# Kernel tuning notes

Measured on AMD Instinct MI355X. Metric: run time of the kernel, lower is better.

## Reference

```python
import jax, jax.numpy as jnp
import numpy as np

N, D, H = 65536, 512, 256  # batch, input_dim, hidden_dim
BN_EPS = 1e-5
EPS = 1e-15


def setup_inputs() -> dict:
    key = jax.random.key(0)
    ks = jax.random.split(key, 10)
    rn = lambda k, shape, sc: jax.random.normal(k, shape, dtype=jnp.float32) * sc
    return {
        "x1": rn(ks[0], (N, D), 1.0),
        "x2": rn(ks[1], (N, D), 1.0),
        "W1": rn(ks[2], (D, H), 0.04),
        "b1": jnp.zeros((H,), jnp.float32),
        "gamma": jnp.ones((H,), jnp.float32),
        "beta_bn": jnp.zeros((H,), jnp.float32),
        "W2": rn(ks[3], (H, H // 2), 0.06),
        "b2": jnp.zeros((H // 2,), jnp.float32),
        "W3": rn(ks[4], (H // 2 * 3, 64), 0.05),
        "b3": jnp.zeros((64,), jnp.float32),
        "W4": rn(ks[5], (64, 1), 0.12),
        "b4": jnp.zeros((1,), jnp.float32),
        "alpha": jnp.array([0.65], jnp.float32),
        "beta": jnp.array([0.25], jnp.float32),
    }


def _proj(x, W1, b1, gamma, beta_bn, W2, b2):
    h = x @ W1 + b1                       # [N, 256]
    mean = jnp.mean(h, axis=0)
    var = jnp.var(h, axis=0)              # biased, matches BN training normalization
    h = gamma * (h - mean) * jax.lax.rsqrt(var + BN_EPS) + beta_bn
    h = jax.nn.relu(h)
    return jax.nn.relu(h @ W2 + b2)       # [N, 128]


def reference(x1, x2, W1, b1, gamma, beta_bn, W2, b2, W3, b3, W4, b4, alpha, beta):
    h1 = _proj(x1, W1, b1, gamma, beta_bn, W2, b2)
    h2 = _proj(x2, W1, b1, gamma, beta_bn, W2, b2)
    # diag of normalized similarity matrix == row-wise cosine similarity
    dot = jnp.sum(h1 * h2, axis=1)
    inv1 = 1.0 / jnp.maximum(jnp.sqrt(jnp.sum(h1 * h1, axis=1)), EPS)
    inv2 = 1.0 / jnp.maximum(jnp.sqrt(jnp.sum(h2 * h2, axis=1)), EPS)
    s_math = jnp.clip(dot * inv1 * inv2, 0.0, 1.0)
    combined = jnp.concatenate([h1 * h2, jnp.abs(h1 - h2), h1 + h2], axis=1)  # [N, 384]
    s_learn = (jax.nn.relu(combined @ W3 + b3) @ W4 + b4).reshape(-1)          # [N]
    final = alpha * s_math + beta * jax.nn.sigmoid(s_learn)
    return jnp.clip(final, 0.0, 1.0)
```

## Files before the change

kernel.cpp:

```cpp
#include <hip/hip_runtime.h>
#include <hip/hip_bf16.h>
#include <math.h>

#define NROWS 65536
#define DIN   512
#define H1    256
#define H2    128
#define K3DIM 384
#define O3    64

typedef short  short8  __attribute__((ext_vector_type(8)));
typedef float  f32x4   __attribute__((ext_vector_type(4)));
typedef unsigned short u16x4 __attribute__((ext_vector_type(4)));

__device__ __forceinline__ unsigned short f2bf(float f) {
    union { float f; unsigned int i; } v; v.f = f;
    unsigned int r = (v.i + 0x7fffu + ((v.i >> 16) & 1u)) >> 16;
    return (unsigned short)r;
}
__device__ __forceinline__ float bf2f(unsigned short u) {
    union { unsigned int i; float f; } v; v.i = ((unsigned int)u) << 16;
    return v.f;
}

typedef const __attribute__((address_space(1))) unsigned int* gas1_t;
typedef __attribute__((address_space(3))) unsigned int* las3_t;
__device__ __forceinline__ void gload_lds16(const void* g, void* l) {
    __builtin_amdgcn_global_load_lds((gas1_t)g, (las3_t)l, 16, 0, 0);
}

__global__ void transpose3_kernel(const float* __restrict__ W1, const float* __restrict__ W2,
                                  const float* __restrict__ W3,
                                  unsigned short* __restrict__ w1t, unsigned short* __restrict__ w2t,
                                  unsigned short* __restrict__ w3t) {
    int idx = blockIdx.x * 256 + threadIdx.x;
    const int n1 = DIN * H1;
    const int n2 = H1 * H2;
    const int n3 = K3DIM * O3;
    if (idx < n1) {
        int c = idx / DIN, r = idx - c * DIN;
        w1t[idx] = f2bf(W1[r * H1 + c]);
    } else if (idx < n1 + n2) {
        int i2 = idx - n1;
        int c = i2 / H1, r = i2 - c * H1;
        w2t[i2] = f2bf(W2[r * H2 + c]);
    } else if (idx < n1 + n2 + n3) {
        int i3 = idx - n1 - n2;
        int c = i3 / K3DIM, r = i3 - c * K3DIM;
        w3t[i3] = f2bf(W3[r * O3 + c]);
    }
}

#define LDA1 32

__global__ __launch_bounds__(256, 2)
void gemm1_kernel(const float* __restrict__ x1, const float* __restrict__ x2,
                  const unsigned short* __restrict__ w1t, const float* __restrict__ b1,
                  unsigned short* __restrict__ h_out, float* __restrict__ stats) {
    __shared__ __align__(1024) unsigned short Al[2][64 * LDA1];
    __shared__ __align__(1024) unsigned short Bl[2][256 * LDA1];
    const int t    = threadIdx.x;
    const int row0 = blockIdx.x * 64;
    const int inp  = row0 >> 16;
    const float* xp = inp ? x2 : x1;
    const int r0 = row0 & (NROWS - 1);

    const int wave = t >> 6, lane = t & 63;
    const int m = lane & 15, q = lane >> 4;

    const int bn_local = lane >> 2;
    const int bk_off   = (lane & 3) * 8;
    const int ar0 = t >> 3;
    const int ak0 = (t & 7) * 4;

    f32x4 acc[4][4] = {};
    float4 va0, va1;

#pragma unroll
    for (int i = 0; i < 4; ++i) {
        int chunk = wave * 4 + i;
        gload_lds16(w1t + (size_t)(chunk * 16 + bn_local) * DIN + bk_off, &Bl[0][chunk * 512]);
    }
    va0 = *reinterpret_cast<const float4*>(xp + (size_t)(r0 + ar0) * DIN + ak0);
    va1 = *reinterpret_cast<const float4*>(xp + (size_t)(r0 + ar0 + 32) * DIN + ak0);
    {
        u16x4 c0; c0.x = f2bf(va0.x); c0.y = f2bf(va0.y); c0.z = f2bf(va0.z); c0.w = f2bf(va0.w);
        u16x4 c1; c1.x = f2bf(va1.x); c1.y = f2bf(va1.y); c1.z = f2bf(va1.z); c1.w = f2bf(va1.w);
        *reinterpret_cast<u16x4*>(&Al[0][ar0 * LDA1 + ak0])        = c0;
        *reinterpret_cast<u16x4*>(&Al[0][(ar0 + 32) * LDA1 + ak0]) = c1;
    }
    __syncthreads();

#pragma unroll
    for (int kt = 0; kt < 16; ++kt) {
        const int d = kt & 1;
        if (kt < 15) {
            const int kn = (kt + 1) * 32;
#pragma unroll
            for (int i = 0; i < 4; ++i) {
                int chunk = wave * 4 + i;
                gload_lds16(w1t + (size_t)(chunk * 16 + bn_local) * DIN + kn + bk_off,
                            &Bl[d ^ 1][chunk * 512]);
            }
            va0 = *reinterpret_cast<const float4*>(xp + (size_t)(r0 + ar0) * DIN + kn + ak0);
            va1 = *reinterpret_cast<const float4*>(xp + (size_t)(r0 + ar0 + 32) * DIN + kn + ak0);
        }
        short8 af[4], bfr[4];
#pragma unroll
        for (int mi = 0; mi < 4; ++mi)
            af[mi] = *reinterpret_cast<const short8*>(&Al[d][(mi * 16 + m) * LDA1 + q * 8]);
#pragma unroll
        for (int ni = 0; ni < 4; ++ni)
            bfr[ni] = *reinterpret_cast<const short8*>(&Bl[d][(wave * 64 + ni * 16 + m) * LDA1 + q * 8]);
#pragma unroll
        for (int mi = 0; mi < 4; ++mi)
#pragma unroll
            for (int ni = 0; ni < 4; ++ni)
                acc[mi][ni] = __builtin_amdgcn_mfma_f32_16x16x32_bf16(af[mi], bfr[ni], acc[mi][ni], 0, 0, 0);
        if (kt < 15) {
            u16x4 c0; c0.x = f2bf(va0.x); c0.y = f2bf(va0.y); c0.z = f2bf(va0.z); c0.w = f2bf(va0.w);
            u16x4 c1; c1.x = f2bf(va1.x); c1.y = f2bf(va1.y); c1.z = f2bf(va1.z); c1.w = f2bf(va1.w);
            *reinterpret_cast<u16x4*>(&Al[d ^ 1][ar0 * LDA1 + ak0])        = c0;
            *reinterpret_cast<u16x4*>(&Al[d ^ 1][(ar0 + 32) * LDA1 + ak0]) = c1;
        }
        __syncthreads();
    }

#pragma unroll
    for (int ni = 0; ni < 4; ++ni) {
        const int col = wave * 64 + ni * 16 + m;
        const float bias = b1[col];
        float s = 0.f, ssq = 0.f;
#pragma unroll
        for (int mi = 0; mi < 4; ++mi) {
#pragma unroll
            for (int r = 0; r < 4; ++r) {
                int row = row0 + mi * 16 + q * 4 + r;
                float v = acc[mi][ni][r] + bias;
                h_out[(size_t)row * H1 + col] = f2bf(v);
                s += v; ssq += v * v;
            }
        }
        s   += __shfl_xor(s, 16);   s   += __shfl_xor(s, 32);
        ssq += __shfl_xor(ssq, 16); ssq += __shfl_xor(ssq, 32);
        if (q == 0) {
            atomicAdd(&stats[(inp * 2 + 0) * H1 + col], s);
            atomicAdd(&stats[(inp * 2 + 1) * H1 + col], ssq);
        }
    }
}

__global__ void bnparams_kernel(const float* __restrict__ stats, const float* __restrict__ gamma,
                                const float* __restrict__ beta_bn, float* __restrict__ ab) {
    int t = threadIdx.x;
    int inp = t >> 8, c = t & 255;
    float mean = stats[(inp * 2 + 0) * H1 + c] * (1.0f / NROWS);
    float ex2  = stats[(inp * 2 + 1) * H1 + c] * (1.0f / NROWS);
    float var  = ex2 - mean * mean;
    float a = gamma[c] * rsqrtf(var + 1e-5f);
    ab[(inp * 2 + 0) * H1 + c] = a;
    ab[(inp * 2 + 1) * H1 + c] = beta_bn[c] - a * mean;
}

#define LDA  40

__global__ __launch_bounds__(256, 2)
void gemm2_kernel(const unsigned short* __restrict__ h, const unsigned short* __restrict__ w2t,
                  const float* __restrict__ b2, const float* __restrict__ ab,
                  unsigned short* __restrict__ z) {
    __shared__ __align__(16) unsigned short Al[2][128 * LDA];
    __shared__ float sc[H1], sh[H1];
    const int t  = threadIdx.x;
    const int m0 = blockIdx.x * 128;
    const int inp = m0 >> 16;
    sc[t] = ab[(inp * 2 + 0) * H1 + t];
    sh[t] = ab[(inp * 2 + 1) * H1 + t];

    const int wave = t >> 6, lane = t & 63;
    const int wm = wave >> 1, wn = wave & 1;
    const int m = lane & 15, q = lane >> 4;
    const int ar = t >> 1, akh = (t & 1) * 16;
    const unsigned short* hrow = h + (size_t)(m0 + ar) * H1 + akh;

    f32x4 acc[4][4] = {};
    short8 bcur[4], bnext[4];
    float4 ha0, ha1;

    ha0 = *reinterpret_cast<const float4*>(hrow);
    ha1 = *reinterpret_cast<const float4*>(hrow + 8);
#pragma unroll
    for (int ni = 0; ni < 4; ++ni)
        bcur[ni] = *reinterpret_cast<const short8*>(w2t + (size_t)(wn * 64 + ni * 16 + m) * H1 + q * 8);
    __syncthreads();
    {
        unsigned short vs[16] __attribute__((aligned(16)));
        unsigned short ob[16] __attribute__((aligned(16)));
        *reinterpret_cast<float4*>(vs)     = ha0;
        *reinterpret_cast<float4*>(vs + 8) = ha1;
#pragma unroll
        for (int j = 0; j < 16; ++j) {
            float v = sc[akh + j] * bf2f(vs[j]) + sh[akh + j];
            ob[j] = f2bf(fmaxf(v, 0.f));
        }
        *reinterpret_cast<float4*>(&Al[0][ar * LDA + akh])     = *reinterpret_cast<float4*>(ob);
        *reinterpret_cast<float4*>(&Al[0][ar * LDA + akh + 8]) = *reinterpret_cast<float4*>(ob + 8);
    }
    __syncthreads();

#pragma unroll
    for (int kt = 0; kt < 8; ++kt) {
        const int d = kt & 1;
        if (kt < 7) {
            const int kn = (kt + 1) * 32;
            ha0 = *reinterpret_cast<const float4*>(hrow + kn);
            ha1 = *reinterpret_cast<const float4*>(hrow + kn + 8);
#pragma unroll
            for (int ni = 0; ni < 4; ++ni)
                bnext[ni] = *reinterpret_cast<const short8*>(
                    w2t + (size_t)(wn * 64 + ni * 16 + m) * H1 + kn + q * 8);
        }
        short8 af[4];
#pragma unroll
        for (int mi = 0; mi < 4; ++mi)
            af[mi] = *reinterpret_cast<const short8*>(&Al[d][(wm * 64 + mi * 16 + m) * LDA + q * 8]);
#pragma unroll
        for (int mi = 0; mi < 4; ++mi)
#pragma unroll
            for (int ni = 0; ni < 4; ++ni)
                acc[mi][ni] = __builtin_amdgcn_mfma_f32_16x16x32_bf16(af[mi], bcur[ni], acc[mi][ni], 0, 0, 0);
        if (kt < 7) {
            const int kn = (kt + 1) * 32;
            unsigned short vs[16] __attribute__((aligned(16)));
            unsigned short ob[16] __attribute__((aligned(16)));
            *reinterpret_cast<float4*>(vs)     = ha0;
            *reinterpret_cast<float4*>(vs + 8) = ha1;
#pragma unroll
            for (int j = 0; j < 16; ++j) {
                int k = kn + akh + j;
                float v = sc[k] * bf2f(vs[j]) + sh[k];
                ob[j] = f2bf(fmaxf(v, 0.f));
            }
            *reinterpret_cast<float4*>(&Al[d ^ 1][ar * LDA + akh])     = *reinterpret_cast<float4*>(ob);
            *reinterpret_cast<float4*>(&Al[d ^ 1][ar * LDA + akh + 8]) = *reinterpret_cast<float4*>(ob + 8);
#pragma unroll
            for (int ni = 0; ni < 4; ++ni) bcur[ni] = bnext[ni];
        }
        __syncthreads();
    }
#pragma unroll
    for (int mi = 0; mi < 4; ++mi)
#pragma unroll
        for (int ni = 0; ni < 4; ++ni) {
            int col = wn * 64 + ni * 16 + m;
            float bias = b2[col];
#pragma unroll
            for (int r = 0; r < 4; ++r) {
                int row = m0 + wm * 64 + mi * 16 + q * 4 + r;
                z[(size_t)row * H2 + col] = f2bf(fmaxf(acc[mi][ni][r] + bias, 0.f));
            }
        }
}

#define LDZ  136

__global__ __launch_bounds__(512, 2)
void head_kernel(const unsigned short* __restrict__ z, const unsigned short* __restrict__ w3t,
                 const float* __restrict__ b3, const float* __restrict__ w4,
                 const float* __restrict__ b4, const float* __restrict__ alpha,
                 const float* __restrict__ beta, float* __restrict__ out) {
    __shared__ __align__(16) unsigned short Z1[128 * LDZ];
    __shared__ __align__(16) unsigned short Z2[128 * LDZ];
    __shared__ float b3s[64], w4s[64];
    __shared__ float smath[128], slearn[128];

    const int t  = threadIdx.x;
    const int r0 = blockIdx.x * 128;

    {
        int r = t >> 2, seg = t & 3;
        const float4* f1 = reinterpret_cast<const float4*>(z + (size_t)(r0 + r) * H2 + seg * 32);
        const float4* f2 = reinterpret_cast<const float4*>(z + (size_t)(NROWS + r0 + r) * H2 + seg * 32);
        float4* d1 = reinterpret_cast<float4*>(&Z1[r * LDZ + seg * 32]);
        float4* d2 = reinterpret_cast<float4*>(&Z2[r * LDZ + seg * 32]);
        d1[0] = f1[0]; d1[1] = f1[1]; d1[2] = f1[2]; d1[3] = f1[3];
        d2[0] = f2[0]; d2[1] = f2[1]; d2[2] = f2[2]; d2[3] = f2[3];
    }
    if (t < 64) { b3s[t] = b3[t]; w4s[t] = w4[t]; }
    __syncthreads();

    {
        int r = t >> 2, part = t & 3;
        float d = 0.f, s1 = 0.f, s2 = 0.f;
#pragma unroll
        for (int j = 0; j < 32; ++j) {
            int k = part * 32 + j;
            float a = bf2f(Z1[r * LDZ + k]);
            float b = bf2f(Z2[r * LDZ + k]);
            d += a * b; s1 += a * a; s2 += b * b;
        }
        d  += __shfl_xor(d, 1);  d  += __shfl_xor(d, 2);
        s1 += __shfl_xor(s1, 1); s1 += __shfl_xor(s1, 2);
        s2 += __shfl_xor(s2, 1); s2 += __shfl_xor(s2, 2);
        if (part == 0) {
            float inv1 = 1.f / fmaxf(sqrtf(s1), 1e-15f);
            float inv2 = 1.f / fmaxf(sqrtf(s2), 1e-15f);
            float sm = d * inv1 * inv2;
            smath[r] = fminf(fmaxf(sm, 0.f), 1.f);
        }
    }

    const int wave = t >> 6, lane = t & 63;
    const int m = lane & 15, q = lane >> 4;
    const int wr = wave * 16;
    f32x4 acc[4] = {};
#pragma unroll
    for (int kb = 0; kb < 12; ++kb) {
        int seg = kb >> 2;
        int kl  = (kb & 3) * 32 + q * 8;
        short8 a1 = *reinterpret_cast<const short8*>(&Z1[(wr + m) * LDZ + kl]);
        short8 a2 = *reinterpret_cast<const short8*>(&Z2[(wr + m) * LDZ + kl]);
        short8 af;
#pragma unroll
        for (int j = 0; j < 8; ++j) {
            float v1 = bf2f((unsigned short)a1[j]);
            float v2 = bf2f((unsigned short)a2[j]);
            float v = (seg == 0) ? v1 * v2 : (seg == 1 ? fabsf(v1 - v2) : v1 + v2);
            af[j] = (short)f2bf(v);
        }
#pragma unroll
        for (int ni = 0; ni < 4; ++ni) {
            short8 bfr = *reinterpret_cast<const short8*>(
                w3t + (size_t)(ni * 16 + m) * K3DIM + kb * 32 + q * 8);
            acc[ni] = __builtin_amdgcn_mfma_f32_16x16x32_bf16(af, bfr, acc[ni], 0, 0, 0);
        }
    }
    float partial[4] = {0.f, 0.f, 0.f, 0.f};
#pragma unroll
    for (int ni = 0; ni < 4; ++ni) {
        int col = ni * 16 + m;
        float bias = b3s[col], w4v = w4s[col];
#pragma unroll
        for (int rg = 0; rg < 4; ++rg) {
            float v = fmaxf(acc[ni][rg] + bias, 0.f);
            partial[rg] += v * w4v;
        }
    }
#pragma unroll
    for (int rg = 0; rg < 4; ++rg) {
        float p = partial[rg];
        p += __shfl_xor(p, 1); p += __shfl_xor(p, 2);
        p += __shfl_xor(p, 4); p += __shfl_xor(p, 8);
        if (m == 0) slearn[wr + q * 4 + rg] = p + b4[0];
    }
    __syncthreads();
    if (t < 128) {
        float sl = slearn[t];
        float sig = 1.f / (1.f + expf(-sl));
        float f = alpha[0] * smath[t] + beta[0] * sig;
        out[r0 + t] = fminf(fmaxf(f, 0.f), 1.f);
    }
}

extern "C" void kernel_launch(void* const* d_in, const int* in_sizes, int n_in,
                              void* d_out, int out_size, void* d_ws, size_t ws_size,
                              hipStream_t stream) {
    (void)in_sizes; (void)n_in; (void)out_size; (void)ws_size;
    const float* x1      = (const float*)d_in[0];
    const float* x2      = (const float*)d_in[1];
    const float* W1      = (const float*)d_in[2];
    const float* b1      = (const float*)d_in[3];
    const float* gamma   = (const float*)d_in[4];
    const float* beta_bn = (const float*)d_in[5];
    const float* W2      = (const float*)d_in[6];
    const float* b2      = (const float*)d_in[7];
    const float* W3      = (const float*)d_in[8];
    const float* b3      = (const float*)d_in[9];
    const float* W4      = (const float*)d_in[10];
    const float* b4      = (const float*)d_in[11];
    const float* alpha   = (const float*)d_in[12];
    const float* beta    = (const float*)d_in[13];
    float* out = (float*)d_out;

    char* ws = (char*)d_ws;
    unsigned short* h   = (unsigned short*)(ws);
    unsigned short* w1t = (unsigned short*)(ws + 67108864);
    unsigned short* w2t = (unsigned short*)(ws + 67371008);
    unsigned short* w3t = (unsigned short*)(ws + 67436544);
    float*          stats = (float*)(ws + 67485696);
    float*          ab    = (float*)(ws + 67489792);
    unsigned short* z   = (unsigned short*)(ws + 67493888);

    (void)hipMemsetAsync(stats, 0, 4096, stream);
    transpose3_kernel<<<(DIN * H1 + H1 * H2 + K3DIM * O3 + 255) / 256, 256, 0, stream>>>(
        W1, W2, W3, w1t, w2t, w3t);
    gemm1_kernel<<<2048, 256, 0, stream>>>(x1, x2, w1t, b1, h, stats);
    bnparams_kernel<<<1, 512, 0, stream>>>(stats, gamma, beta_bn, ab);
    gemm2_kernel<<<1024, 256, 0, stream>>>(h, w2t, b2, ab, z);
    head_kernel<<<512, 512, 0, stream>>>(z, w3t, b3, W4, b4, alpha, beta, out);
}
```

Before: 420.5 us.

## Use single-buffered BK=64 tiles with XOR-swizzled LDS for gemm1 and gemm2

Both GEMMs drop register/LDS double buffering and instead stage 64-wide K tiles in one LDS buffer, with two syncs per tile. B tiles are loaded directly into LDS through global_load_lds with an XOR swizzle to avoid bank conflicts. gemm2 now also stages W2 through LDS rather than reading it from global memory into registers. This halves the number of K iterations and cuts bank conflicts, but it gives up overlap of loads with MFMA work inside a block and relies on the two blocks per CU to hide latency.

```diff
diff --git a/kernel.cpp b/kernel.cpp
--- a/kernel.cpp
+++ b/kernel.cpp
@@ -11,7 +11,6 @@
 
 typedef short  short8  __attribute__((ext_vector_type(8)));
 typedef float  f32x4   __attribute__((ext_vector_type(4)));
-typedef unsigned short u16x4 __attribute__((ext_vector_type(4)));
 
 __device__ __forceinline__ unsigned short f2bf(float f) {
     union { float f; unsigned int i; } v; v.f = f;
@@ -51,84 +50,78 @@
     }
 }
 
-#define LDA1 32
+#define LDA1P 72
 
 __global__ __launch_bounds__(256, 2)
 void gemm1_kernel(const float* __restrict__ x1, const float* __restrict__ x2,
                   const unsigned short* __restrict__ w1t, const float* __restrict__ b1,
                   unsigned short* __restrict__ h_out, float* __restrict__ stats) {
-    __shared__ __align__(1024) unsigned short Al[2][64 * LDA1];
-    __shared__ __align__(1024) unsigned short Bl[2][256 * LDA1];
+    __shared__ __align__(1024) unsigned short Bl[256 * 64];
+    __shared__ __align__(16)   unsigned short Al[64 * LDA1P];
     const int t    = threadIdx.x;
     const int row0 = blockIdx.x * 64;
     const int inp  = row0 >> 16;
     const float* xp = inp ? x2 : x1;
     const int r0 = row0 & (NROWS - 1);
 
-    const int wave = t >> 6, lane = t & 63;
+    const int w = t >> 6, lane = t & 63;
     const int m = lane & 15, q = lane >> 4;
 
-    const int bn_local = lane >> 2;
-    const int bk_off   = (lane & 3) * 8;
-    const int ar0 = t >> 3;
-    const int ak0 = (t & 7) * 4;
+    const int brow_l = lane >> 3;
+    const int bslot  = (lane & 7) ^ brow_l;
+    const int arow  = t >> 2;
+    const int akseg = (t & 3) * 16;
 
     f32x4 acc[4][4] = {};
-    float4 va0, va1;
-
-#pragma unroll
-    for (int i = 0; i < 4; ++i) {
-        int chunk = wave * 4 + i;
-        gload_lds16(w1t + (size_t)(chunk * 16 + bn_local) * DIN + bk_off, &Bl[0][chunk * 512]);
-    }
-    va0 = *reinterpret_cast<const float4*>(xp + (size_t)(r0 + ar0) * DIN + ak0);
-    va1 = *reinterpret_cast<const float4*>(xp + (size_t)(r0 + ar0 + 32) * DIN + ak0);
-    {
-        u16x4 c0; c0.x = f2bf(va0.x); c0.y = f2bf(va0.y); c0.z = f2bf(va0.z); c0.w = f2bf(va0.w);
-        u16x4 c1; c1.x = f2bf(va1.x); c1.y = f2bf(va1.y); c1.z = f2bf(va1.z); c1.w = f2bf(va1.w);
-        *reinterpret_cast<u16x4*>(&Al[0][ar0 * LDA1 + ak0])        = c0;
-        *reinterpret_cast<u16x4*>(&Al[0][(ar0 + 32) * LDA1 + ak0]) = c1;
-    }
-    __syncthreads();
-
-#pragma unroll
-    for (int kt = 0; kt < 16; ++kt) {
-        const int d = kt & 1;
-        if (kt < 15) {
-            const int kn = (kt + 1) * 32;
-#pragma unroll
-            for (int i = 0; i < 4; ++i) {
-                int chunk = wave * 4 + i;
-                gload_lds16(w1t + (size_t)(chunk * 16 + bn_local) * DIN + kn + bk_off,
-                            &Bl[d ^ 1][chunk * 512]);
-            }
-            va0 = *reinterpret_cast<const float4*>(xp + (size_t)(r0 + ar0) * DIN + kn + ak0);
-            va1 = *reinterpret_cast<const float4*>(xp + (size_t)(r0 + ar0 + 32) * DIN + kn + ak0);
-        }
-        short8 af[4], bfr[4];
-#pragma unroll
-        for (int mi = 0; mi < 4; ++mi)
-            af[mi] = *reinterpret_cast<const short8*>(&Al[d][(mi * 16 + m) * LDA1 + q * 8]);
-#pragma unroll
-        for (int ni = 0; ni < 4; ++ni)
-            bfr[ni] = *reinterpret_cast<const short8*>(&Bl[d][(wave * 64 + ni * 16 + m) * LDA1 + q * 8]);
-#pragma unroll
-        for (int mi = 0; mi < 4; ++mi)
-#pragma unroll
-            for (int ni = 0; ni < 4; ++ni)
-                acc[mi][ni] = __builtin_amdgcn_mfma_f32_16x16x32_bf16(af[mi], bfr[ni], acc[mi][ni], 0, 0, 0);
-        if (kt < 15) {
-            u16x4 c0; c0.x = f2bf(va0.x); c0.y = f2bf(va0.y); c0.z = f2bf(va0.z); c0.w = f2bf(va0.w);
-            u16x4 c1; c1.x = f2bf(va1.x); c1.y = f2bf(va1.y); c1.z = f2bf(va1.z); c1.w = f2bf(va1.w);
-            *reinterpret_cast<u16x4*>(&Al[d ^ 1][ar0 * LDA1 + ak0])        = c0;
-            *reinterpret_cast<u16x4*>(&Al[d ^ 1][(ar0 + 32) * LDA1 + ak0]) = c1;
-        }
+
+    for (int kt = 0; kt < 8; ++kt) {
+        const int k0 = kt * 64;
         __syncthreads();
+#pragma unroll
+        for (int i = 0; i < 8; ++i) {
+            int c = w * 8 + i;
+            gload_lds16(w1t + (size_t)(c * 8 + brow_l) * DIN + k0 + bslot * 8,
+                        &Bl[c * 512]);
+        }
+        {
+            const float* asrc = xp + (size_t)(r0 + arow) * DIN + k0 + akseg;
+            float4 v0 = *reinterpret_cast<const float4*>(asrc);
+            float4 v1 = *reinterpret_cast<const float4*>(asrc + 4);
+            float4 v2 = *reinterpret_cast<const float4*>(asrc + 8);
+            float4 v3 = *reinterpret_cast<const float4*>(asrc + 12);
+            unsigned short ob[16] __attribute__((aligned(16)));
+            ob[0]=f2bf(v0.x); ob[1]=f2bf(v0.y); ob[2]=f2bf(v0.z); ob[3]=f2bf(v0.w);
+            ob[4]=f2bf(v1.x); ob[5]=f2bf(v1.y); ob[6]=f2bf(v1.z); ob[7]=f2bf(v1.w);
+            ob[8]=f2bf(v2.x); ob[9]=f2bf(v2.y); ob[10]=f2bf(v2.z); ob[11]=f2bf(v2.w);
+            ob[12]=f2bf(v3.x); ob[13]=f2bf(v3.y); ob[14]=f2bf(v3.z); ob[15]=f2bf(v3.w);
+            *reinterpret_cast<float4*>(&Al[arow * LDA1P + akseg])     = *reinterpret_cast<float4*>(ob);
+            *reinterpret_cast<float4*>(&Al[arow * LDA1P + akseg + 8]) = *reinterpret_cast<float4*>(ob + 8);
+        }
+        __syncthreads();
+#pragma unroll
+        for (int s = 0; s < 2; ++s) {
+            short8 af[4], bfr[4];
+#pragma unroll
+            for (int mi = 0; mi < 4; ++mi)
+                af[mi] = *reinterpret_cast<const short8*>(&Al[(mi * 16 + m) * LDA1P + s * 32 + q * 8]);
+#pragma unroll
+            for (int ni = 0; ni < 4; ++ni) {
+                int rb = w * 64 + ni * 16 + m;
+                int kb = (q * 16 + s * 64) ^ ((m & 7) << 4);
+                bfr[ni] = *reinterpret_cast<const short8*>(
+                    reinterpret_cast<const char*>(Bl) + rb * 128 + kb);
+            }
+#pragma unroll
+            for (int mi = 0; mi < 4; ++mi)
+#pragma unroll
+                for (int ni = 0; ni < 4; ++ni)
+                    acc[mi][ni] = __builtin_amdgcn_mfma_f32_16x16x32_bf16(af[mi], bfr[ni], acc[mi][ni], 0, 0, 0);
+        }
     }
 
 #pragma unroll
     for (int ni = 0; ni < 4; ++ni) {
-        const int col = wave * 64 + ni * 16 + m;
+        const int col = w * 64 + ni * 16 + m;
         const float bias = b1[col];
         float s = 0.f, ssq = 0.f;
 #pragma unroll
@@ -162,13 +155,12 @@
     ab[(inp * 2 + 1) * H1 + c] = beta_bn[c] - a * mean;
 }
 
-#define LDA  40
-
 __global__ __launch_bounds__(256, 2)
 void gemm2_kernel(const unsigned short* __restrict__ h, const unsigned short* __restrict__ w2t,
                   const float* __restrict__ b2, const float* __restrict__ ab,
                   unsigned short* __restrict__ z) {
-    __shared__ __align__(16) unsigned short Al[2][128 * LDA];
+    __shared__ __align__(1024) unsigned short B2l[128 * 64];
+    __shared__ __align__(16)   unsigned short A2l[128 * LDA1P];
     __shared__ float sc[H1], sh[H1];
     const int t  = threadIdx.x;
     const int m0 = blockIdx.x * 128;
@@ -176,76 +168,66 @@
     sc[t] = ab[(inp * 2 + 0) * H1 + t];
     sh[t] = ab[(inp * 2 + 1) * H1 + t];
 
-    const int wave = t >> 6, lane = t & 63;
-    const int wm = wave >> 1, wn = wave & 1;
+    const int w = t >> 6, lane = t & 63;
+    const int wm = w >> 1, wn = w & 1;
     const int m = lane & 15, q = lane >> 4;
-    const int ar = t >> 1, akh = (t & 1) * 16;
-    const unsigned short* hrow = h + (size_t)(m0 + ar) * H1 + akh;
+
+    const int brow_l = lane >> 3;
+    const int bslot  = (lane & 7) ^ brow_l;
+    const int arow  = t >> 1;
+    const int akseg = (t & 1) * 32;
 
     f32x4 acc[4][4] = {};
-    short8 bcur[4], bnext[4];
-    float4 ha0, ha1;
-
-    ha0 = *reinterpret_cast<const float4*>(hrow);
-    ha1 = *reinterpret_cast<const float4*>(hrow + 8);
-#pragma unroll
-    for (int ni = 0; ni < 4; ++ni)
-        bcur[ni] = *reinterpret_cast<const short8*>(w2t + (size_t)(wn * 64 + ni * 16 + m) * H1 + q * 8);
-    __syncthreads();
-    {
-        unsigned short vs[16] __attribute__((aligned(16)));
-        unsigned short ob[16] __attribute__((aligned(16)));
-        *reinterpret_cast<float4*>(vs)     = ha0;
-        *reinterpret_cast<float4*>(vs + 8) = ha1;
-#pragma unroll
-        for (int j = 0; j < 16; ++j) {
-            float v = sc[akh + j] * bf2f(vs[j]) + sh[akh + j];
-            ob[j] = f2bf(fmaxf(v, 0.f));
-        }
-        *reinterpret_cast<float4*>(&Al[0][ar * LDA + akh])     = *reinterpret_cast<float4*>(ob);
-        *reinterpret_cast<float4*>(&Al[0][ar * LDA + akh + 8]) = *reinterpret_cast<float4*>(ob + 8);
-    }
-    __syncthreads();
-
-#pragma unroll
-    for (int kt = 0; kt < 8; ++kt) {
-        const int d = kt & 1;
-        if (kt < 7) {
-            const int kn = (kt + 1) * 32;
-            ha0 = *reinterpret_cast<const float4*>(hrow + kn);
-            ha1 = *reinterpret_cast<const float4*>(hrow + kn + 8);
-#pragma unroll
-            for (int ni = 0; ni < 4; ++ni)
-                bnext[ni] = *reinterpret_cast<const short8*>(
-                    w2t + (size_t)(wn * 64 + ni * 16 + m) * H1 + kn + q * 8);
-        }
-        short8 af[4];
-#pragma unroll
-        for (int mi = 0; mi < 4; ++mi)
-            af[mi] = *reinterpret_cast<const short8*>(&Al[d][(wm * 64 + mi * 16 + m) * LDA + q * 8]);
-#pragma unroll
-        for (int mi = 0; mi < 4; ++mi)
-#pragma unroll
-            for (int ni = 0; ni < 4; ++ni)
-                acc[mi][ni] = __builtin_amdgcn_mfma_f32_16x16x32_bf16(af[mi], bcur[ni], acc[mi][ni], 0, 0, 0);
-        if (kt < 7) {
-            const int kn = (kt + 1) * 32;
-            unsigned short vs[16] __attribute__((aligned(16)));
-            unsigned short ob[16] __attribute__((aligned(16)));
-            *reinterpret_cast<float4*>(vs)     = ha0;
-            *reinterpret_cast<float4*>(vs + 8) = ha1;
-#pragma unroll
-            for (int j = 0; j < 16; ++j) {
-                int k = kn + akh + j;
-                float v = sc[k] * bf2f(vs[j]) + sh[k];
-                ob[j] = f2bf(fmaxf(v, 0.f));
-            }
-            *reinterpret_cast<float4*>(&Al[d ^ 1][ar * LDA + akh])     = *reinterpret_cast<float4*>(ob);
-            *reinterpret_cast<float4*>(&Al[d ^ 1][ar * LDA + akh + 8]) = *reinterpret_cast<float4*>(ob + 8);
-#pragma unroll
-            for (int ni = 0; ni < 4; ++ni) bcur[ni] = bnext[ni];
-        }
+
+    for (int kt = 0; kt < 4; ++kt) {
+        const int k0 = kt * 64;
         __syncthreads();
+#pragma unroll
+        for (int i = 0; i < 4; ++i) {
+            int c = w * 4 + i;
+            gload_lds16(w2t + (size_t)(c * 8 + brow_l) * H1 + k0 + bslot * 8,
+                        &B2l[c * 512]);
+        }
+        {
+            const unsigned short* asrc = h + (size_t)(m0 + arow) * H1 + k0 + akseg;
+            short8 v0 = *reinterpret_cast<const short8*>(asrc);
+            short8 v1 = *reinterpret_cast<const short8*>(asrc + 8);
+            short8 v2 = *reinterpret_cast<const short8*>(asrc + 16);
+            short8 v3 = *reinterpret_cast<const short8*>(asrc + 24);
+            unsigned short ob[32] __attribute__((aligned(16)));
+#pragma unroll
+            for (int j = 0; j < 8; ++j) {
+                int k = k0 + akseg + j;
+                ob[j]      = f2bf(fmaxf(sc[k]      * bf2f((unsigned short)v0[j]) + sh[k],      0.f));
+                ob[j + 8]  = f2bf(fmaxf(sc[k + 8]  * bf2f((unsigned short)v1[j]) + sh[k + 8],  0.f));
+                ob[j + 16] = f2bf(fmaxf(sc[k + 16] * bf2f((unsigned short)v2[j]) + sh[k + 16], 0.f));
+                ob[j + 24] = f2bf(fmaxf(sc[k + 24] * bf2f((unsigned short)v3[j]) + sh[k + 24], 0.f));
+            }
+#pragma unroll
+            for (int i = 0; i < 4; ++i)
+                *reinterpret_cast<float4*>(&A2l[arow * LDA1P + akseg + i * 8]) =
+                    *reinterpret_cast<float4*>(ob + i * 8);
+        }
+        __syncthreads();
+#pragma unroll
+        for (int s = 0; s < 2; ++s) {
+            short8 af[4], bfr[4];
+#pragma unroll
+            for (int mi = 0; mi < 4; ++mi)
+                af[mi] = *reinterpret_cast<const short8*>(&A2l[(wm * 64 + mi * 16 + m) * LDA1P + s * 32 + q * 8]);
+#pragma unroll
+            for (int ni = 0; ni < 4; ++ni) {
+                int rb = wn * 64 + ni * 16 + m;
+                int kb = (q * 16 + s * 64) ^ ((m & 7) << 4);
+                bfr[ni] = *reinterpret_cast<const short8*>(
+                    reinterpret_cast<const char*>(B2l) + rb * 128 + kb);
+            }
+#pragma unroll
+            for (int mi = 0; mi < 4; ++mi)
+#pragma unroll
+                for (int ni = 0; ni < 4; ++ni)
+                    acc[mi][ni] = __builtin_amdgcn_mfma_f32_16x16x32_bf16(af[mi], bfr[ni], acc[mi][ni], 0, 0, 0);
+        }
     }
 #pragma unroll
     for (int mi = 0; mi < 4; ++mi)
```

Result: faster. 377.5 us (-10.2%).
